# Kernel tuning notes

Measured on AMD Instinct MI355X. Metric: run time of the kernel, lower is better.

The kernel has to match this reference:

```python
import jax, jax.numpy as jnp
import numpy as np
from jax import lax

SEQ, B, F, L = 32, 32, 64, 256
OC = 128          # out_channels
K = 5
PAD = (K - 1) // 2
GROUPS = 4 * OC // 32  # GroupNorm groups = 16
EPS = 1e-5


def group_norm(x, w, b):
    # x: (B, C, L); normalize over each group's (C//G, L) slice
    bsz, c, l = x.shape
    xg = x.reshape(bsz, GROUPS, -1)
    mu = jnp.mean(xg, axis=-1, keepdims=True)
    var = jnp.var(xg, axis=-1, keepdims=True)
    xg = (xg - mu) * lax.rsqrt(var + EPS)
    return xg.reshape(bsz, c, l) * w[None, :, None] + b[None, :, None]


def setup_inputs() -> dict:
    key = jax.random.key(0)
    k1, k2, k3 = jax.random.split(key, 3)
    fan_in = (F + OC) * K
    return {
        "inputs": jax.random.normal(k1, (SEQ, B, F, L), dtype=jnp.float32),
        "conv_w": jax.random.normal(k2, (4 * OC, F + OC, K), dtype=jnp.float32) / np.sqrt(fan_in),
        "conv_b": jax.random.normal(k3, (4 * OC,), dtype=jnp.float32) * 0.01,
        "gn_w": jnp.ones((4 * OC,), dtype=jnp.float32),
        "gn_b": jnp.zeros((4 * OC,), dtype=jnp.float32),
    }


def reference(inputs, conv_w, conv_b, gn_w, gn_b):
    bsz, sub_len = inputs.shape[1], inputs.shape[3]
    hx0 = jnp.zeros((bsz, OC, sub_len), dtype=inputs.dtype)
    cx0 = jnp.zeros((bsz, OC, sub_len), dtype=inputs.dtype)

    def step(carry, x):
        hx, cx = carry
        combined = jnp.concatenate([x, hx], axis=1)  # (B, F+OC, L)
        gates = lax.conv_general_dilated(
            combined, conv_w, window_strides=(1,), padding=[(PAD, PAD)],
            dimension_numbers=("NCH", "OIH", "NCH"))
        gates = gates + conv_b[None, :, None]
        gates = group_norm(gates, gn_w, gn_b)
        i, f, g, o = jnp.split(gates, 4, axis=1)
        cy = jax.nn.sigmoid(f) * cx + jax.nn.sigmoid(i) * jnp.tanh(g)
        hy = jax.nn.sigmoid(o) * jnp.tanh(cy)
        return (hy, cy), hy

    (hy, cy), outputs = lax.scan(step, (hx0, cx0), inputs)
    return outputs, (hy, cy)
```

## Files before the change

### kernel.cpp

```cpp
#include <hip/hip_runtime.h>

typedef unsigned short u16;
typedef unsigned int u32;
typedef unsigned long long u64;
typedef __attribute__((ext_vector_type(4))) float f32x4;
typedef __attribute__((ext_vector_type(8))) short s16x8;
typedef __attribute__((ext_vector_type(4))) int i32x4;

#define EPS 1e-5f

__device__ __forceinline__ u16 f2bf(float f) {
  unsigned u = __float_as_uint(f);
  return (u16)((u + 0x7fffu + ((u >> 16) & 1u)) >> 16);
}
__device__ __forceinline__ float sigm(float x) { return 1.0f / (1.0f + __expf(-x)); }
__device__ __forceinline__ float tanh_f(float x) {
  float e = __expf(-2.0f * fabsf(x));
  float r = (1.0f - e) / (1.0f + e);
  return copysignf(r, x);
}
__device__ __forceinline__ void gl_lds16(const void* g, void* l) {
  __builtin_amdgcn_global_load_lds(
      (const __attribute__((address_space(1))) u32*)g,
      (__attribute__((address_space(3))) u32*)l, 16, 0, 0);
}

__global__ __launch_bounds__(256) void k_setup(
    const float* __restrict__ cw, u16* __restrict__ Wpk,
    const float* __restrict__ x, u16* __restrict__ xT,
    i32x4* __restrict__ hTz, i32x4* __restrict__ cxz) {
  const int bid = blockIdx.x, tid = threadIdx.x;
  __shared__ __align__(16) u16 ltile[256 * 72];
  if (bid < 1920) {
    int idx = bid * 256 + tid;
    int f = idx >> 9, r = idx & 511;
    int lane = r >> 3, j = r & 7;
    int of = f & 31, tk = f >> 5;
    int kk = tk % 6, tap = tk / 6;
    int o = (of << 4) + (lane & 15);
    int c = (kk << 5) + ((lane >> 4) << 3) + j;
    Wpk[idx] = f2bf(cw[(o * 192 + c) * 5 + tap]);
  } else if (bid < 2944) {
    int tb = bid - 1920;
    const float* src = x + tb * (64 * 256);
    for (int it = 0; it < 64; ++it) {
      int idx = it * 256 + tid;
      int c = idx >> 8, l = idx & 255;
      ltile[l * 72 + c] = f2bf(src[idx]);
    }
    __syncthreads();
    char* dst = (char*)(xT + tb * 16896);
    i32x4 z = {0, 0, 0, 0};
    for (int i = tid; i < 2112; i += 256) {
      int r = i >> 3, ch = i & 7;
      i32x4 v = z;
      if (r >= 2 && r < 258) v = *(const i32x4*)(ltile + (r - 2) * 72 + ch * 8);
      *(i32x4*)(dst + r * 128 + ((ch * 16) ^ ((r & 7) << 4))) = v;
    }
  } else {
    int base = (bid - 2944) * 256 + tid;
    i32x4 z = {0, 0, 0, 0};
    for (int i = base; i < 270336; i += 131072) hTz[i] = z;
    for (int i = base; i < 262144; i += 131072) cxz[i] = z;
  }
}

__global__ __launch_bounds__(512, 1) void k_step(
    const u16* __restrict__ Wpk, const u16* __restrict__ xT, u16* __restrict__ hT,
    const float* __restrict__ cb, const float* __restrict__ gnw, const float* __restrict__ gnb,
    float* __restrict__ cx, float* __restrict__ out, int t) {
  const int bid = blockIdx.x;
  const int b = bid & 31, cs = bid >> 5;
  const int tid = threadIdx.x, wave = tid >> 6, lane = tid & 63;
  const int wm = wave & 1, wl = wave >> 1;
  const int l15 = lane & 15, q = lane >> 4;
  const int cgrp = q << 4;

  __shared__ __align__(16) char ldsx[33792];
  __shared__ __align__(16) char ldsh[67584];
  __shared__ __align__(16) char hl[16384];
  __shared__ float red[8][4][2];
  __shared__ float smu[4], srs[4];

  const u16* hTr = hT + (t & 1) * 1081344;
  u16* hTw = hT + ((t + 1) & 1) * 1081344;

  {
    const char* gx = (const char*)(xT + ((t << 5) + b) * 16896);
    for (int i = tid; i < 2112; i += 512) gl_lds16(gx + (i << 4), ldsx + (i << 4));
    const char* gh = (const char*)hTr + b * 67584;
    for (int i = tid; i < 4224; i += 512) gl_lds16(gh + (i << 4), ldsh + (i << 4));
  }
  asm volatile("s_waitcnt vmcnt(0)" ::: "memory");
  __syncthreads();

  f32x4 zero4 = {0.f, 0.f, 0.f, 0.f};
  f32x4 acc[4][4];
  #pragma unroll
  for (int g = 0; g < 4; ++g)
    #pragma unroll
    for (int ni = 0; ni < 4; ++ni) acc[g][ni] = zero4;

  const s16x8* Wv = (const s16x8*)Wpk;
  for (int tap = 0; tap < 5; ++tap) {
    #pragma unroll
    for (int kk = 0; kk < 6; ++kk) {
      const int cc = tap * 6 + kk;
      s16x8 av[4], bv[4];
      #pragma unroll
      for (int g = 0; g < 4; ++g) {
        const int of = (g << 3) + (cs << 1) + wm;
        av[g] = Wv[(((cc << 5) + of) << 6) + lane];
      }
      #pragma unroll
      for (int ni = 0; ni < 4; ++ni) {
        const int rr = (wl << 6) + (ni << 4) + l15 + tap;
        const int sw = (rr & 7) << 4;
        bv[ni] = (kk < 2)
          ? *(const s16x8*)(ldsx + (rr << 7) + (((kk << 6) + cgrp) ^ sw))
          : *(const s16x8*)(ldsh + (rr << 8) + ((((kk - 2) << 6) + cgrp) ^ sw));
      }
      #pragma unroll
      for (int g = 0; g < 4; ++g)
        #pragma unroll
        for (int ni = 0; ni < 4; ++ni)
          acc[g][ni] = __builtin_amdgcn_mfma_f32_16x16x32_bf16(av[g], bv[ni], acc[g][ni], 0, 0, 0);
    }
  }

  const int chq = (cs << 5) + (wm << 4) + (q << 2);
  float sum4[4], sq4[4];
  #pragma unroll
  for (int g = 0; g < 4; ++g) {
    const f32x4 bias = *(const f32x4*)(cb + (g << 7) + chq);
    sum4[g] = 0.f; sq4[g] = 0.f;
    #pragma unroll
    for (int ni = 0; ni < 4; ++ni)
      #pragma unroll
      for (int r = 0; r < 4; ++r) {
        float v = acc[g][ni][r] + bias[r];
        acc[g][ni][r] = v;
        sum4[g] += v; sq4[g] += v * v;
      }
  }
  f32x4 w4[4], b4[4];
  float cxv[4][4];
  #pragma unroll
  for (int g = 0; g < 4; ++g) {
    w4[g] = *(const f32x4*)(gnw + (g << 7) + chq);
    b4[g] = *(const f32x4*)(gnb + (g << 7) + chq);
  }
  #pragma unroll
  for (int ni = 0; ni < 4; ++ni) {
    const int l = (wl << 6) + (ni << 4) + l15;
    #pragma unroll
    for (int r = 0; r < 4; ++r)
      cxv[ni][r] = cx[(b << 15) + ((chq + r) << 8) + l];
  }
  #pragma unroll
  for (int off = 1; off < 64; off <<= 1) {
    #pragma unroll
    for (int g = 0; g < 4; ++g) {
      sum4[g] += __shfl_xor(sum4[g], off);
      sq4[g]  += __shfl_xor(sq4[g], off);
    }
  }
  if (lane == 0) {
    #pragma unroll
    for (int g = 0; g < 4; ++g) { red[wave][g][0] = sum4[g]; red[wave][g][1] = sq4[g]; }
  }
  __syncthreads();
  if (tid < 4) {
    float s = 0.f, qv = 0.f;
    #pragma unroll
    for (int w = 0; w < 8; ++w) { s += red[w][tid][0]; qv += red[w][tid][1]; }
    const float inv = 1.0f / 8192.0f;
    float m = s * inv;
    smu[tid] = m;
    srs[tid] = rsqrtf(qv * inv - m * m + EPS);
  }
  __syncthreads();

  const float mu0 = smu[0], mu1 = smu[1], mu2 = smu[2], mu3 = smu[3];
  const float rs0 = srs[0], rs1 = srs[1], rs2 = srs[2], rs3 = srs[3];
  float* outp = out + (((t << 5) + b) << 15);
  #pragma unroll
  for (int ni = 0; ni < 4; ++ni) {
    const int l = (wl << 6) + (ni << 4) + l15;
    u16 hp[4];
    #pragma unroll
    for (int r = 0; r < 4; ++r) {
      const int c = chq + r;
      float vi = (acc[0][ni][r] - mu0) * rs0 * w4[0][r] + b4[0][r];
      float vf = (acc[1][ni][r] - mu1) * rs1 * w4[1][r] + b4[1][r];
      float vg = (acc[2][ni][r] - mu2) * rs2 * w4[2][r] + b4[2][r];
      float vo = (acc[3][ni][r] - mu3) * rs3 * w4[3][r] + b4[3][r];
      float cyv = sigm(vf) * cxv[ni][r] + sigm(vi) * tanh_f(vg);
      float hyv = sigm(vo) * tanh_f(cyv);
      const int ci = (c << 8) + l;
      cx[(b << 15) + ci] = cyv;
      outp[ci] = hyv;
      hp[r] = f2bf(hyv);
      if (t == 31) {
        out[33554432 + (b << 15) + ci] = hyv;
        out[34603008 + (b << 15) + ci] = cyv;
      }
    }
    *(u64*)(hl + (l << 6) + (((wm << 5) + (q << 3)) ^ ((l & 3) << 4))) =
        *(const u64*)hp;
  }
  __syncthreads();

  #pragma unroll
  for (int i = tid; i < 1024; i += 512) {
    const int ll = i >> 2, k = i & 3;
    const int row = ll + 2;
    i32x4 v = *(const i32x4*)(hl + (ll << 6) + ((k << 4) ^ ((ll & 3) << 4)));
    char* dst = (char*)hTw + b * 67584 + (row << 8) +
                ((((cs << 2) + k) << 4) ^ ((row & 7) << 4));
    *(i32x4*)dst = v;
  }
}

extern "C" void kernel_launch(void* const* d_in, const int* in_sizes, int n_in,
                              void* d_out, int out_size, void* d_ws, size_t ws_size,
                              hipStream_t stream) {
  const float* x  = (const float*)d_in[0];
  const float* cw = (const float*)d_in[1];
  const float* cb = (const float*)d_in[2];
  const float* gw = (const float*)d_in[3];
  const float* gb = (const float*)d_in[4];
  float* out = (float*)d_out;
  char* ws = (char*)d_ws;

  u16*   Wpk = (u16*)(ws);
  u16*   xT  = (u16*)(ws + 983040);
  u16*   hT  = (u16*)(ws + 35586048);
  float* cx  = (float*)(ws + 39911424);

  k_setup<<<3456, 256, 0, stream>>>(cw, Wpk, x, xT, (i32x4*)hT, (i32x4*)cx);
  for (int t = 0; t < 32; ++t)
    k_step<<<128, 512, 0, stream>>>(Wpk, xT, hT, cb, gw, gb, cx, out, t);
}
```

Baseline: 707.6 us.

## Fuse timestep launches into persistent kernel with per-batch flag synchronization

Result: slower. 1.156 ms (+63.4%).

```diff
diff --git a/kernel.cpp b/kernel.cpp
--- a/kernel.cpp
+++ b/kernel.cpp
@@ -27,8 +27,7 @@
 
 __global__ __launch_bounds__(256) void k_setup(
     const float* __restrict__ cw, u16* __restrict__ Wpk,
-    const float* __restrict__ x, u16* __restrict__ xT,
-    i32x4* __restrict__ hTz, i32x4* __restrict__ cxz) {
+    const float* __restrict__ x, u16* __restrict__ xT, int* __restrict__ flags) {
   const int bid = blockIdx.x, tid = threadIdx.x;
   __shared__ __align__(16) u16 ltile[256 * 72];
   if (bid < 1920) {
@@ -58,17 +57,16 @@
       *(i32x4*)(dst + r * 128 + ((ch * 16) ^ ((r & 7) << 4))) = v;
     }
   } else {
-    int base = (bid - 2944) * 256 + tid;
-    i32x4 z = {0, 0, 0, 0};
-    for (int i = base; i < 270336; i += 131072) hTz[i] = z;
-    for (int i = base; i < 262144; i += 131072) cxz[i] = z;
-  }
-}
-
-__global__ __launch_bounds__(512, 1) void k_step(
-    const u16* __restrict__ Wpk, const u16* __restrict__ xT, u16* __restrict__ hT,
+    int i = (bid - 2944) * 256 + tid;
+    #pragma unroll
+    for (int k = 0; k < 4; ++k) flags[(k << 11) + i] = 0;
+  }
+}
+
+__global__ __launch_bounds__(512, 2) void k_mega(
+    const u16* __restrict__ Wpk, const u16* __restrict__ xT,
     const float* __restrict__ cb, const float* __restrict__ gnw, const float* __restrict__ gnb,
-    float* __restrict__ cx, float* __restrict__ out, int t) {
+    float* __restrict__ out, u32* __restrict__ hA, int* __restrict__ flags) {
   const int bid = blockIdx.x;
   const int b = bid & 31, cs = bid >> 5;
   const int tid = threadIdx.x, wave = tid >> 6, lane = tid & 63;
@@ -78,147 +76,179 @@
 
   __shared__ __align__(16) char ldsx[33792];
   __shared__ __align__(16) char ldsh[67584];
-  __shared__ __align__(16) char hl[16384];
   __shared__ float red[8][4][2];
   __shared__ float smu[4], srs[4];
 
-  const u16* hTr = hT + (t & 1) * 1081344;
-  u16* hTw = hT + ((t + 1) & 1) * 1081344;
+  const int chq = (cs << 5) + (wm << 4) + (q << 2);
+  f32x4 biasv[4], w4[4], b4[4];
+  #pragma unroll
+  for (int g = 0; g < 4; ++g) {
+    biasv[g] = *(const f32x4*)(cb  + (g << 7) + chq);
+    w4[g]    = *(const f32x4*)(gnw + (g << 7) + chq);
+    b4[g]    = *(const f32x4*)(gnb + (g << 7) + chq);
+  }
+  float cxr[4][4];
+  #pragma unroll
+  for (int ni = 0; ni < 4; ++ni)
+    #pragma unroll
+    for (int r = 0; r < 4; ++r) cxr[ni][r] = 0.f;
 
   {
-    const char* gx = (const char*)(xT + ((t << 5) + b) * 16896);
+    i32x4 z = {0, 0, 0, 0};
+    for (int i = tid; i < 4224; i += 512) ((i32x4*)ldsh)[i] = z;
+    const char* gx = (const char*)(xT + b * 16896);
     for (int i = tid; i < 2112; i += 512) gl_lds16(gx + (i << 4), ldsx + (i << 4));
-    const char* gh = (const char*)hTr + b * 67584;
-    for (int i = tid; i < 4224; i += 512) gl_lds16(gh + (i << 4), ldsh + (i << 4));
   }
   asm volatile("s_waitcnt vmcnt(0)" ::: "memory");
   __syncthreads();
 
-  f32x4 zero4 = {0.f, 0.f, 0.f, 0.f};
-  f32x4 acc[4][4];
-  #pragma unroll
-  for (int g = 0; g < 4; ++g)
-    #pragma unroll
-    for (int ni = 0; ni < 4; ++ni) acc[g][ni] = zero4;
-
   const s16x8* Wv = (const s16x8*)Wpk;
-  for (int tap = 0; tap < 5; ++tap) {
-    #pragma unroll
-    for (int kk = 0; kk < 6; ++kk) {
-      const int cc = tap * 6 + kk;
-      s16x8 av[4], bv[4];
+
+  #pragma unroll 1
+  for (int t = 0; t < 32; ++t) {
+    f32x4 zero4 = {0.f, 0.f, 0.f, 0.f};
+    f32x4 acc[4][4];
+    #pragma unroll
+    for (int g = 0; g < 4; ++g)
+      #pragma unroll
+      for (int ni = 0; ni < 4; ++ni) acc[g][ni] = zero4;
+
+    for (int tap = 0; tap < 5; ++tap) {
+      #pragma unroll
+      for (int kk = 0; kk < 6; ++kk) {
+        const int cc = tap * 6 + kk;
+        s16x8 av[4], bv[4];
+        #pragma unroll
+        for (int g = 0; g < 4; ++g) {
+          const int of = (g << 3) + (cs << 1) + wm;
+          av[g] = Wv[(((cc << 5) + of) << 6) + lane];
+        }
+        #pragma unroll
+        for (int ni = 0; ni < 4; ++ni) {
+          const int rr = (wl << 6) + (ni << 4) + l15 + tap;
+          const int sw = (rr & 7) << 4;
+          bv[ni] = (kk < 2)
+            ? *(const s16x8*)(ldsx + (rr << 7) + (((kk << 6) + cgrp) ^ sw))
+            : *(const s16x8*)(ldsh + (rr << 8) + ((((kk - 2) << 6) + cgrp) ^ sw));
+        }
+        #pragma unroll
+        for (int g = 0; g < 4; ++g)
+          #pragma unroll
+          for (int ni = 0; ni < 4; ++ni)
+            acc[g][ni] = __builtin_amdgcn_mfma_f32_16x16x32_bf16(av[g], bv[ni], acc[g][ni], 0, 0, 0);
+      }
+    }
+    __syncthreads();
+
+    float sum4[4], sq4[4];
+    #pragma unroll
+    for (int g = 0; g < 4; ++g) {
+      sum4[g] = 0.f; sq4[g] = 0.f;
+      #pragma unroll
+      for (int ni = 0; ni < 4; ++ni)
+        #pragma unroll
+        for (int r = 0; r < 4; ++r) {
+          float v = acc[g][ni][r] + biasv[g][r];
+          acc[g][ni][r] = v;
+          sum4[g] += v; sq4[g] += v * v;
+        }
+    }
+    #pragma unroll
+    for (int off = 1; off < 64; off <<= 1) {
       #pragma unroll
       for (int g = 0; g < 4; ++g) {
-        const int of = (g << 3) + (cs << 1) + wm;
-        av[g] = Wv[(((cc << 5) + of) << 6) + lane];
-      }
-      #pragma unroll
-      for (int ni = 0; ni < 4; ++ni) {
-        const int rr = (wl << 6) + (ni << 4) + l15 + tap;
-        const int sw = (rr & 7) << 4;
-        bv[ni] = (kk < 2)
-          ? *(const s16x8*)(ldsx + (rr << 7) + (((kk << 6) + cgrp) ^ sw))
-          : *(const s16x8*)(ldsh + (rr << 8) + ((((kk - 2) << 6) + cgrp) ^ sw));
-      }
-      #pragma unroll
-      for (int g = 0; g < 4; ++g)
-        #pragma unroll
-        for (int ni = 0; ni < 4; ++ni)
-          acc[g][ni] = __builtin_amdgcn_mfma_f32_16x16x32_bf16(av[g], bv[ni], acc[g][ni], 0, 0, 0);
-    }
-  }
-
-  const int chq = (cs << 5) + (wm << 4) + (q << 2);
-  float sum4[4], sq4[4];
-  #pragma unroll
-  for (int g = 0; g < 4; ++g) {
-    const f32x4 bias = *(const f32x4*)(cb + (g << 7) + chq);
-    sum4[g] = 0.f; sq4[g] = 0.f;
-    #pragma unroll
-    for (int ni = 0; ni < 4; ++ni)
+        sum4[g] += __shfl_xor(sum4[g], off);
+        sq4[g]  += __shfl_xor(sq4[g], off);
+      }
+    }
+    if (lane == 0) {
+      #pragma unroll
+      for (int g = 0; g < 4; ++g) { red[wave][g][0] = sum4[g]; red[wave][g][1] = sq4[g]; }
+    }
+    __syncthreads();
+    if (tid < 4) {
+      float s = 0.f, qv = 0.f;
+      #pragma unroll
+      for (int w = 0; w < 8; ++w) { s += red[w][tid][0]; qv += red[w][tid][1]; }
+      const float inv = 1.0f / 8192.0f;
+      float m = s * inv;
+      smu[tid] = m;
+      srs[tid] = rsqrtf(qv * inv - m * m + EPS);
+    }
+    __syncthreads();
+
+    const float mu0 = smu[0], mu1 = smu[1], mu2 = smu[2], mu3 = smu[3];
+    const float rs0 = srs[0], rs1 = srs[1], rs2 = srs[2], rs3 = srs[3];
+    const int cur = t & 1;
+    u32* hAme = hA + (((cur << 5) | b) << 14) + (cs << 12);
+    float* outp = out + (((t << 5) + b) << 15);
+    #pragma unroll
+    for (int ni = 0; ni < 4; ++ni) {
+      const int l = (wl << 6) + (ni << 4) + l15;
+      u16 hp[4];
       #pragma unroll
       for (int r = 0; r < 4; ++r) {
-        float v = acc[g][ni][r] + bias[r];
-        acc[g][ni][r] = v;
-        sum4[g] += v; sq4[g] += v * v;
-      }
-  }
-  f32x4 w4[4], b4[4];
-  float cxv[4][4];
-  #pragma unroll
-  for (int g = 0; g < 4; ++g) {
-    w4[g] = *(const f32x4*)(gnw + (g << 7) + chq);
-    b4[g] = *(const f32x4*)(gnb + (g << 7) + chq);
-  }
-  #pragma unroll
-  for (int ni = 0; ni < 4; ++ni) {
-    const int l = (wl << 6) + (ni << 4) + l15;
-    #pragma unroll
-    for (int r = 0; r < 4; ++r)
-      cxv[ni][r] = cx[(b << 15) + ((chq + r) << 8) + l];
-  }
-  #pragma unroll
-  for (int off = 1; off < 64; off <<= 1) {
-    #pragma unroll
-    for (int g = 0; g < 4; ++g) {
-      sum4[g] += __shfl_xor(sum4[g], off);
-      sq4[g]  += __shfl_xor(sq4[g], off);
-    }
-  }
-  if (lane == 0) {
-    #pragma unroll
-    for (int g = 0; g < 4; ++g) { red[wave][g][0] = sum4[g]; red[wave][g][1] = sq4[g]; }
-  }
-  __syncthreads();
-  if (tid < 4) {
-    float s = 0.f, qv = 0.f;
-    #pragma unroll
-    for (int w = 0; w < 8; ++w) { s += red[w][tid][0]; qv += red[w][tid][1]; }
-    const float inv = 1.0f / 8192.0f;
-    float m = s * inv;
-    smu[tid] = m;
-    srs[tid] = rsqrtf(qv * inv - m * m + EPS);
-  }
-  __syncthreads();
-
-  const float mu0 = smu[0], mu1 = smu[1], mu2 = smu[2], mu3 = smu[3];
-  const float rs0 = srs[0], rs1 = srs[1], rs2 = srs[2], rs3 = srs[3];
-  float* outp = out + (((t << 5) + b) << 15);
-  #pragma unroll
-  for (int ni = 0; ni < 4; ++ni) {
-    const int l = (wl << 6) + (ni << 4) + l15;
-    u16 hp[4];
-    #pragma unroll
-    for (int r = 0; r < 4; ++r) {
-      const int c = chq + r;
-      float vi = (acc[0][ni][r] - mu0) * rs0 * w4[0][r] + b4[0][r];
-      float vf = (acc[1][ni][r] - mu1) * rs1 * w4[1][r] + b4[1][r];
-      float vg = (acc[2][ni][r] - mu2) * rs2 * w4[2][r] + b4[2][r];
-      float vo = (acc[3][ni][r] - mu3) * rs3 * w4[3][r] + b4[3][r];
-      float cyv = sigm(vf) * cxv[ni][r] + sigm(vi) * tanh_f(vg);
-      float hyv = sigm(vo) * tanh_f(cyv);
-      const int ci = (c << 8) + l;
-      cx[(b << 15) + ci] = cyv;
-      outp[ci] = hyv;
-      hp[r] = f2bf(hyv);
-      if (t == 31) {
-        out[33554432 + (b << 15) + ci] = hyv;
-        out[34603008 + (b << 15) + ci] = cyv;
-      }
-    }
-    *(u64*)(hl + (l << 6) + (((wm << 5) + (q << 3)) ^ ((l & 3) << 4))) =
-        *(const u64*)hp;
-  }
-  __syncthreads();
-
-  #pragma unroll
-  for (int i = tid; i < 1024; i += 512) {
-    const int ll = i >> 2, k = i & 3;
-    const int row = ll + 2;
-    i32x4 v = *(const i32x4*)(hl + (ll << 6) + ((k << 4) ^ ((ll & 3) << 4)));
-    char* dst = (char*)hTw + b * 67584 + (row << 8) +
-                ((((cs << 2) + k) << 4) ^ ((row & 7) << 4));
-    *(i32x4*)dst = v;
+        const int c = chq + r;
+        float vi = (acc[0][ni][r] - mu0) * rs0 * w4[0][r] + b4[0][r];
+        float vf = (acc[1][ni][r] - mu1) * rs1 * w4[1][r] + b4[1][r];
+        float vg = (acc[2][ni][r] - mu2) * rs2 * w4[2][r] + b4[2][r];
+        float vo = (acc[3][ni][r] - mu3) * rs3 * w4[3][r] + b4[3][r];
+        float cyv = sigm(vf) * cxr[ni][r] + sigm(vi) * tanh_f(vg);
+        float hyv = sigm(vo) * tanh_f(cyv);
+        cxr[ni][r] = cyv;
+        const int ci = (c << 8) + l;
+        outp[ci] = hyv;
+        hp[r] = f2bf(hyv);
+        if (t == 31) {
+          out[33554432 + (b << 15) + ci] = hyv;
+          out[34603008 + (b << 15) + ci] = cyv;
+        }
+      }
+      const int row = l + 2;
+      const int bo = (cs << 6) + (wm << 5) + (q << 3);
+      *(u64*)(ldsh + (row << 8) + (((bo >> 4) << 4) ^ ((row & 7) << 4)) + (bo & 15)) =
+          *(const u64*)hp;
+      if (t < 31) {
+        const int u = (wm << 3) + (q << 1);
+        __hip_atomic_store(hAme + (u << 8) + l, (u32)hp[0] | ((u32)hp[1] << 16),
+                           __ATOMIC_RELAXED, __HIP_MEMORY_SCOPE_AGENT);
+        __hip_atomic_store(hAme + ((u + 1) << 8) + l, (u32)hp[2] | ((u32)hp[3] << 16),
+                           __ATOMIC_RELAXED, __HIP_MEMORY_SCOPE_AGENT);
+      }
+    }
+
+    if (t < 31) {
+      asm volatile("s_waitcnt vmcnt(0)" ::: "memory");
+      __syncthreads();
+      if (tid == 0)
+        __hip_atomic_store(flags + (bid << 6), t + 1, __ATOMIC_RELAXED, __HIP_MEMORY_SCOPE_AGENT);
+      {
+        const char* gx = (const char*)(xT + (((t + 1) << 5) + b) * 16896);
+        for (int i = tid; i < 2112; i += 512) gl_lds16(gx + (i << 4), ldsx + (i << 4));
+      }
+      if (tid < 3) {
+        const int pcs = tid + (tid >= cs ? 1 : 0);
+        int* pf = flags + (((pcs << 5) | b) << 6);
+        while (__hip_atomic_load(pf, __ATOMIC_RELAXED, __HIP_MEMORY_SCOPE_AGENT) <= t)
+          __builtin_amdgcn_s_sleep(2);
+      }
+      __syncthreads();
+      #pragma unroll
+      for (int pj = 0; pj < 3; ++pj) {
+        const int pcs = pj + (pj >= cs ? 1 : 0);
+        const u32* src = hA + (((cur << 5) | b) << 14) + (pcs << 12);
+        #pragma unroll
+        for (int j = 0; j < 8; ++j) {
+          const int idx = (j << 9) + tid;
+          u32 v = __hip_atomic_load(src + idx, __ATOMIC_RELAXED, __HIP_MEMORY_SCOPE_AGENT);
+          const int u = idx >> 8, l = idx & 255, row = l + 2;
+          const int bo = (pcs << 6) + (u << 2);
+          *(u32*)(ldsh + (row << 8) + (((bo >> 4) << 4) ^ ((row & 7) << 4)) + (bo & 15)) = v;
+        }
+      }
+      asm volatile("s_waitcnt vmcnt(0)" ::: "memory");
+      __syncthreads();
+    }
   }
 }
 
@@ -233,12 +263,11 @@
   float* out = (float*)d_out;
   char* ws = (char*)d_ws;
 
-  u16*   Wpk = (u16*)(ws);
-  u16*   xT  = (u16*)(ws + 983040);
-  u16*   hT  = (u16*)(ws + 35586048);
-  float* cx  = (float*)(ws + 39911424);
-
-  k_setup<<<3456, 256, 0, stream>>>(cw, Wpk, x, xT, (i32x4*)hT, (i32x4*)cx);
-  for (int t = 0; t < 32; ++t)
-    k_step<<<128, 512, 0, stream>>>(Wpk, xT, hT, cb, gw, gb, cx, out, t);
-}
+  u16* Wpk   = (u16*)(ws);
+  u16* xT    = (u16*)(ws + 983040);
+  u32* hA    = (u32*)(ws + 35586048);
+  int* flags = (int*)(ws + 39780352);
+
+  k_setup<<<2952, 256, 0, stream>>>(cw, Wpk, x, xT, flags);
+  k_mega<<<128, 512, 0, stream>>>(Wpk, xT, cb, gw, gb, out, hA, flags);
+}
```
